# Optimization experiments

Hardware: AMD Instinct MI355X
Metric: run time of the kernel (lower is better)

The kernel has to match this reference:

```python
import jax, jax.numpy as jnp
import numpy as np

K = 9  # knn kernel_size
SLOPE = 0.01  # LeakyReLU slope inside EdgeConv MLP (PyGraphBipartite default)


def setup_inputs() -> dict:
    key = jax.random.key(0)
    ks = jax.random.split(key, 5)
    B, C, H, W = 8, 96, 64, 64
    x = jax.random.normal(ks[0], (B, C, H, W), dtype=jnp.float32)
    # EdgeConv MLP: Linear(2C -> C), LeakyReLU(0.01), Linear(C -> C)
    W1 = jax.random.normal(ks[1], (2 * C, C), dtype=jnp.float32) * (1.0 / np.sqrt(2 * C))
    b1 = jax.random.normal(ks[2], (C,), dtype=jnp.float32) * 0.01
    W2 = jax.random.normal(ks[3], (C, C), dtype=jnp.float32) * (1.0 / np.sqrt(C))
    b2 = jax.random.normal(ks[4], (C,), dtype=jnp.float32) * 0.01
    return {"x": x, "W1": W1, "b1": b1, "W2": W2, "b2": b2}


def reference(x, W1, b1, W2, b2):
    B, C, H, W = x.shape
    M = H * W
    # flat_nodes: (B,C,H,W) -> per-image node features (B, M, C)
    xf = jnp.transpose(x, (0, 2, 3, 1)).reshape(B, M, C)

    # k-NN graph per image (batch-restricted), loop=True so self is a neighbor (dist 0)
    sq = jnp.sum(xf * xf, axis=-1)  # (B, M)
    dist = sq[:, :, None] + sq[:, None, :] - 2.0 * jnp.einsum("bmc,bnc->bmn", xf, xf)
    _, idx = jax.lax.top_k(-dist, K)  # (B, M, K) neighbor indices per center node

    # gather neighbor features: (B, M, K, C)
    xj = jax.vmap(lambda f, i: f[i])(xf, idx)
    xi = xf[:, :, None, :]  # center node, broadcast over K

    # EdgeConv message: MLP([x_i ; x_j - x_i]), then mean over neighbors
    feat = jnp.concatenate([jnp.broadcast_to(xi, xj.shape), xj - xi], axis=-1)  # (B,M,K,2C)
    h = feat @ W1 + b1
    h = jnp.where(h >= 0, h, SLOPE * h)  # LeakyReLU(0.01)
    h = h @ W2 + b2  # (B, M, K, C)
    out = jnp.mean(h, axis=2)  # mean aggregation -> (B, M, C)

    # norm='none' (Identity), act='relu'
    out = jax.nn.relu(out)

    # unflat_nodes: (B, M, C) -> (B, C, H, W)
    return jnp.transpose(out.reshape(B, H, W, C), (0, 3, 1, 2))
```

## Files before the change

### kernel.cpp

```cpp
#include <hip/hip_runtime.h>

#define B_ 8
#define C_ 96
#define CP_ 104
#define M_ 4096
#define K_ 9
#define NSPLIT 2
#define NPART (M_ / NSPLIT)
#define NTILES (NPART / 64)

typedef _Float16 f16x8 __attribute__((ext_vector_type(8)));
typedef float f32x4 __attribute__((ext_vector_type(4)));

#define INSERT(dv, nv) do {                                                   \
    const int pz_ = tpos;                                                     \
    _Pragma("unroll")                                                         \
    for (int k_ = 0; k_ < K_; ++k_) if (k_ == pz_) { tv[k_] = (dv); ti[k_] = (nv); } \
    float mx_ = tv[0]; int mp_ = 0;                                           \
    _Pragma("unroll")                                                         \
    for (int k_ = 1; k_ < K_; ++k_) if (tv[k_] > mx_) { mx_ = tv[k_]; mp_ = k_; } \
    tmax = mx_; tpos = mp_;                                                   \
  } while (0)

__global__ __launch_bounds__(256) void prep1_kernel(
    const float* __restrict__ x, float* __restrict__ sq,
    unsigned short* __restrict__ xhi, unsigned short* __restrict__ xlo) {
  __shared__ float Xt[C_][64];
  const int b = blockIdx.y, m0 = blockIdx.x * 64, tid = threadIdx.x;
  const float* xb = x + (size_t)b * C_ * M_;
  for (int i = tid; i < C_ * 16; i += 256) {
    int c = i >> 4, j4 = (i & 15) << 2;
    *(float4*)&Xt[c][j4] = *(const float4*)&xb[(size_t)c * M_ + m0 + j4];
  }
  __syncthreads();
  if (tid < 64) {
    float s = 0.f;
#pragma unroll
    for (int c = 0; c < C_; ++c) { float v = Xt[c][tid]; s += v * v; }
    sq[b * M_ + m0 + tid] = s;
  }
  const int p = tid & 63, part = tid >> 6;
  union { unsigned short u[24]; uint4 q[3]; } hb, lb;
#pragma unroll
  for (int i = 0; i < 24; ++i) {
    float v = Xt[part * 24 + i][p];
    _Float16 h = (_Float16)v;
    _Float16 l = (_Float16)(v - (float)h);
    hb.u[i] = __builtin_bit_cast(unsigned short, h);
    lb.u[i] = __builtin_bit_cast(unsigned short, l);
  }
  size_t base = ((size_t)b * M_ + m0 + p) * CP_ + part * 24;
#pragma unroll
  for (int i = 0; i < 3; ++i) {
    *(uint4*)&xhi[base + i * 8] = hb.q[i];
    *(uint4*)&xlo[base + i * 8] = lb.q[i];
  }
}

__global__ __launch_bounds__(256, 3) void knn_kernel(
    const unsigned short* __restrict__ xhi, const unsigned short* __restrict__ xlo,
    const float* __restrict__ sq, float* __restrict__ pv, int* __restrict__ pi) {
  __shared__ struct { unsigned short bhi[64 * CP_]; unsigned short blo[64 * CP_]; } S;
  __shared__ float sqc[64];
  const int b = blockIdx.y, r0 = blockIdx.x * 64, h = blockIdx.z;
  const int tid = threadIdx.x;
  const int lane = tid & 63, w = tid >> 6;
  const int fp = lane & 15, kg = lane >> 4;
  const size_t bm = (size_t)b * M_;
  const int nbeg = h * NPART;

  f16x8 qhi[3], qlo[3];
#pragma unroll
  for (int kt = 0; kt < 3; ++kt) {
    size_t off = (bm + r0 + w * 16 + fp) * CP_ + kt * 32 + kg * 8;
    qhi[kt] = *(const f16x8*)&xhi[off];
    qlo[kt] = *(const f16x8*)&xlo[off];
  }

  float tv[K_]; int ti[K_]; float tmax = 3.4e38f; int tpos = 0;
#pragma unroll
  for (int k = 0; k < K_; ++k) { tv[k] = 3.4e38f; ti[k] = 0; }

  uint4 ph0, ph1, ph2, ph3, pl0, pl1, pl2, pl3;
  float sqreg = 0.f;
  auto gload = [&](int n0) {
    const uint4* gh = (const uint4*)(xhi + (bm + n0) * CP_);
    const uint4* gl = (const uint4*)(xlo + (bm + n0) * CP_);
    ph0 = gh[tid]; ph1 = gh[tid + 256]; ph2 = gh[tid + 512];
    pl0 = gl[tid]; pl1 = gl[tid + 256]; pl2 = gl[tid + 512];
    if (tid < 64) {
      ph3 = gh[tid + 768]; pl3 = gl[tid + 768];
      sqreg = sq[bm + n0 + tid];
    }
  };
  auto swrite = [&]() {
    uint4* dh = (uint4*)S.bhi; uint4* dl = (uint4*)S.blo;
    dh[tid] = ph0; dh[tid + 256] = ph1; dh[tid + 512] = ph2;
    dl[tid] = pl0; dl[tid + 256] = pl1; dl[tid + 512] = pl2;
    if (tid < 64) { dh[tid + 768] = ph3; dl[tid + 768] = pl3; sqc[tid] = sqreg; }
  };

  gload(nbeg);
  for (int t = 0; t < NTILES; ++t) {
    const int n0 = nbeg + t * 64;
    __syncthreads();
    swrite();
    if (t < NTILES - 1) gload(n0 + 64);
    __syncthreads();

    float b0d = 0.f, b1d = 0.f; int b0n = 0, b1n = 0, bcnt = 0;

#pragma unroll
    for (int rs = 0; rs < 4; ++rs) {
      f16x8 nh[3], nl[3];
#pragma unroll
      for (int kt = 0; kt < 3; ++kt) {
        int boff = (rs * 16 + fp) * CP_ + kt * 32 + kg * 8;
        nh[kt] = *(const f16x8*)&S.bhi[boff];
        nl[kt] = *(const f16x8*)&S.blo[boff];
      }
      f32x4 acc = {0.f, 0.f, 0.f, 0.f};
#pragma unroll
      for (int kt = 0; kt < 3; ++kt) {
        acc = __builtin_amdgcn_mfma_f32_16x16x32_f16(nh[kt], qhi[kt], acc, 0, 0, 0);
        acc = __builtin_amdgcn_mfma_f32_16x16x32_f16(nh[kt], qlo[kt], acc, 0, 0, 0);
        acc = __builtin_amdgcn_mfma_f32_16x16x32_f16(nl[kt], qhi[kt], acc, 0, 0, 0);
      }
#pragma unroll
      for (int r = 0; r < 4; ++r) {
        const int nrow = rs * 16 + kg * 4 + r;
        const float d = sqc[nrow] - 2.f * acc[r];
        if (d < tmax) {
          const int n = n0 + nrow;
          if (bcnt == 2) {
            if (b0d < tmax) INSERT(b0d, b0n);
            b0d = b1d; b0n = b1n;
            b1d = d;   b1n = n;
          } else if (bcnt == 1) {
            b1d = d; b1n = n; bcnt = 2;
          } else {
            b0d = d; b0n = n; bcnt = 1;
          }
        }
      }
    }
    if (bcnt >= 1 && b0d < tmax) INSERT(b0d, b0n);
    if (bcnt == 2 && b1d < tmax) INSERT(b1d, b1n);
  }

  __syncthreads();
  float* mv = (float*)&S;
  int*   mi = (int*)((char*)&S + 64 * 37 * 4);
  const int qrow = w * 16 + fp;
#pragma unroll
  for (int k = 0; k < K_; ++k) {
    mv[qrow * 37 + kg * K_ + k] = tv[k];
    mi[qrow * 37 + kg * K_ + k] = ti[k];
  }
  __syncthreads();
  if (tid < 64) {
    float fv[K_]; int fi[K_];
    float mx = 3.4e38f; int mp = 0;
#pragma unroll
    for (int k = 0; k < K_; ++k) { fv[k] = 3.4e38f; fi[k] = 0; }
    for (int s = 0; s < 36; ++s) {
      float v = mv[tid * 37 + s]; int id = mi[tid * 37 + s];
      if (v < mx) {
#pragma unroll
        for (int k = 0; k < K_; ++k) if (k == mp) { fv[k] = v; fi[k] = id; }
        float m2 = fv[0]; int p2 = 0;
#pragma unroll
        for (int k = 1; k < K_; ++k) if (fv[k] > m2) { m2 = fv[k]; p2 = k; }
        mx = m2; mp = p2;
      }
    }
    size_t base = ((size_t)h * B_ * M_ + bm + r0 + tid) * K_;
#pragma unroll
    for (int k = 0; k < K_; ++k) { pv[base + k] = fv[k]; pi[base + k] = fi[k]; }
  }
}

__global__ __launch_bounds__(256) void knn_merge_kernel(
    const float* __restrict__ pv, const int* __restrict__ pi,
    int* __restrict__ idxw) {
  const int g = blockIdx.x * 256 + threadIdx.x;
  float tv[K_]; int ti[K_]; float tmax = 3.4e38f; int tpos = 0;
#pragma unroll
  for (int k = 0; k < K_; ++k) { tv[k] = 3.4e38f; ti[k] = 0; }
#pragma unroll
  for (int h = 0; h < NSPLIT; ++h) {
    const float* vs = pv + ((size_t)h * B_ * M_ + g) * K_;
    const int*   is = pi + ((size_t)h * B_ * M_ + g) * K_;
#pragma unroll
    for (int s = 0; s < K_; ++s) {
      float d = vs[s];
      if (d < tmax) { int n = is[s]; INSERT(d, n); }
    }
  }
#pragma unroll
  for (int k = 0; k < K_; ++k) idxw[(size_t)g * K_ + k] = ti[k];
}

__global__ __launch_bounds__(256) void prep2_kernel(
    const float* __restrict__ x, const float* __restrict__ W1,
    const float* __restrict__ b1, float* __restrict__ P, float* __restrict__ Q) {
  __shared__ float Xt[C_][64];
  __shared__ float Wt[C_][64];
  const int b = blockIdx.y, m0 = blockIdx.x * 64;
  const int tid = threadIdx.x;
  const float* xb = x + (size_t)b * C_ * M_;

  for (int i = tid; i < C_ * 16; i += 256) {
    int c = i >> 4, j4 = (i & 15) << 2;
    *(float4*)&Xt[c][j4] = *(const float4*)&xb[(size_t)c * M_ + m0 + j4];
  }

  const int ty = tid >> 4, tx = tid & 15;
  for (int t = 0; t < 3; ++t) {
    const int u0 = t * 64;
    __syncthreads();
    for (int i = tid; i < C_ * 64; i += 256) {
      int cin = i >> 6, j = i & 63;
      int u = u0 + j;
      float wv;
      if (u < C_) wv = W1[cin * C_ + u] - W1[(C_ + cin) * C_ + u];
      else        wv = W1[(C_ + cin) * C_ + (u - C_)];
      Wt[cin][j] = wv;
    }
    __syncthreads();
    float acc[4][4] = {};
#pragma unroll 8
    for (int c = 0; c < C_; ++c) {
      float4 rr = *(const float4*)&Xt[c][ty << 2];
      float4 ww = *(const float4*)&Wt[c][tx << 2];
      acc[0][0] += rr.x * ww.x; acc[0][1] += rr.x * ww.y; acc[0][2] += rr.x * ww.z; acc[0][3] += rr.x * ww.w;
      acc[1][0] += rr.y * ww.x; acc[1][1] += rr.y * ww.y; acc[1][2] += rr.y * ww.z; acc[1][3] += rr.y * ww.w;
      acc[2][0] += rr.z * ww.x; acc[2][1] += rr.z * ww.y; acc[2][2] += rr.z * ww.z; acc[2][3] += rr.z * ww.w;
      acc[3][0] += rr.w * ww.x; acc[3][1] += rr.w * ww.y; acc[3][2] += rr.w * ww.z; acc[3][3] += rr.w * ww.w;
    }
#pragma unroll
    for (int i = 0; i < 4; ++i) {
      int m = m0 + (ty << 2) + i;
      size_t base = ((size_t)b * M_ + m) * C_;
#pragma unroll
      for (int j = 0; j < 4; ++j) {
        int u = u0 + (tx << 2) + j;
        float v = acc[i][j];
        if (u < C_) P[base + u] = v + b1[u];
        else        Q[base + (u - C_)] = v;
      }
    }
  }
}

__global__ __launch_bounds__(256) void edge_mlp_kernel(
    const float* __restrict__ P, const float* __restrict__ Q,
    const int* __restrict__ idxw, const float* __restrict__ W2,
    const float* __restrict__ b2, float* __restrict__ out) {
  __shared__ float g_l[C_][64];
  __shared__ float W2t[C_ * C_];
  const int b = blockIdx.y, m0 = blockIdx.x * 64;
  const int tid = threadIdx.x;

  for (int i = tid; i < (C_ * C_) / 4; i += 256)
    *(float4*)&W2t[i * 4] = *(const float4*)&W2[i * 4];

  const int ml = tid & 63, cg = tid >> 6;
  const int m = m0 + ml;
  const float* prow = P + ((size_t)b * M_ + m) * C_ + cg * 24;
  float pr[24];
#pragma unroll
  for (int t = 0; t < 24; t += 4) {
    float4 v = *(const float4*)(prow + t);
    pr[t] = v.x; pr[t + 1] = v.y; pr[t + 2] = v.z; pr[t + 3] = v.w;
  }
  float gacc[24] = {};
  const int* irow = idxw + ((size_t)b * M_ + m) * K_;
#pragma unroll
  for (int k = 0; k < K_; ++k) {
    int j = irow[k];
    const float* qrow = Q + ((size_t)b * M_ + j) * C_ + cg * 24;
#pragma unroll
    for (int t = 0; t < 24; t += 4) {
      float4 qv = *(const float4*)(qrow + t);
      float h;
      h = pr[t + 0] + qv.x; gacc[t + 0] += (h >= 0.f) ? h : 0.01f * h;
      h = pr[t + 1] + qv.y; gacc[t + 1] += (h >= 0.f) ? h : 0.01f * h;
      h = pr[t + 2] + qv.z; gacc[t + 2] += (h >= 0.f) ? h : 0.01f * h;
      h = pr[t + 3] + qv.w; gacc[t + 3] += (h >= 0.f) ? h : 0.01f * h;
    }
  }
#pragma unroll
  for (int t = 0; t < 24; ++t) g_l[cg * 24 + t][ml] = gacc[t] * (1.f / 9.f);
  __syncthreads();

  const int ty = tid >> 4, tx = tid & 15;
  float acc2[4][6] = {};
#pragma unroll 4
  for (int c = 0; c < C_; ++c) {
    float4 rr = *(const float4*)&g_l[c][ty << 2];
    float2 wa = *(const float2*)&W2t[c * C_ + tx * 6];
    float2 wb = *(const float2*)&W2t[c * C_ + tx * 6 + 2];
    float2 wc = *(const float2*)&W2t[c * C_ + tx * 6 + 4];
    float rv[4] = {rr.x, rr.y, rr.z, rr.w};
    float wv[6] = {wa.x, wa.y, wb.x, wb.y, wc.x, wc.y};
#pragma unroll
    for (int i = 0; i < 4; ++i)
#pragma unroll
      for (int j = 0; j < 6; ++j) acc2[i][j] += rv[i] * wv[j];
  }
#pragma unroll
  for (int i = 0; i < 4; ++i) {
    int mm = m0 + (ty << 2) + i;
#pragma unroll
    for (int j = 0; j < 6; ++j) {
      int u = tx * 6 + j;
      float v = acc2[i][j] + b2[u];
      v = fmaxf(v, 0.f);
      out[((size_t)b * C_ + u) * M_ + mm] = v;
    }
  }
}

extern "C" void kernel_launch(void* const* d_in, const int* in_sizes, int n_in,
                              void* d_out, int out_size, void* d_ws, size_t ws_size,
                              hipStream_t stream) {
  const float* x  = (const float*)d_in[0];
  const float* W1 = (const float*)d_in[1];
  const float* b1 = (const float*)d_in[2];
  const float* W2 = (const float*)d_in[3];
  const float* b2 = (const float*)d_in[4];
  float* out = (float*)d_out;

  char* ws = (char*)d_ws;
  float* sq  = (float*)ws;
  int* idxw  = (int*)(ws + 131072);
  unsigned short* xhi = (unsigned short*)(ws + 1310720);
  unsigned short* xlo = (unsigned short*)(ws + 8126464);
  float* pv = (float*)(ws + 14942208);
  int*   pi = (int*)(ws + 19660800);
  float* P = (float*)(ws + 1310720);
  float* Q = (float*)(ws + 13893632);

  dim3 blk(256);
  prep1_kernel<<<dim3(M_ / 64, B_), blk, 0, stream>>>(x, sq, xhi, xlo);
  knn_kernel<<<dim3(M_ / 64, B_, NSPLIT), blk, 0, stream>>>(xhi, xlo, sq, pv, pi);
  knn_merge_kernel<<<dim3(B_ * M_ / 256), blk, 0, stream>>>(pv, pi, idxw);
  prep2_kernel<<<dim3(M_ / 64, B_), blk, 0, stream>>>(x, W1, b1, P, Q);
  edge_mlp_kernel<<<dim3(M_ / 64, B_), blk, 0, stream>>>(P, Q, idxw, W2, b2, out);
}
```

Before: 278.5 us.

## Split kNN candidate range four ways and use branchless top-2 filtering per tile

Splits the candidate range into four parts instead of two, which doubles the block count for the distance/top-k kernel and raises parallelism. Each tile's per-row selection is also reworked: every lane branchlessly tracks its two smallest distances and counts how many fall below the current threshold. Only when some lane has more than two qualifying candidates does the wave fall back to full insertion over the stored distances. This cuts divergent insertion work in the common case, at the cost of more partial lists to merge and extra registers for the 16 stored distances.

```diff
diff --git a/kernel.cpp b/kernel.cpp
--- a/kernel.cpp
+++ b/kernel.cpp
@@ -5,7 +5,7 @@
 #define CP_ 104
 #define M_ 4096
 #define K_ 9
-#define NSPLIT 2
+#define NSPLIT 4
 #define NPART (M_ / NSPLIT)
 #define NTILES (NPART / 64)
 
@@ -108,7 +108,10 @@
     if (t < NTILES - 1) gload(n0 + 64);
     __syncthreads();
 
-    float b0d = 0.f, b1d = 0.f; int b0n = 0, b1n = 0, bcnt = 0;
+    const float t0 = tmax;
+    float s0 = 3.4e38f, s1 = 3.4e38f;
+    int i0 = 0, i1 = 0, cnt = 0;
+    float dstore[16];
 
 #pragma unroll
     for (int rs = 0; rs < 4; ++rs) {
@@ -129,23 +132,35 @@
 #pragma unroll
       for (int r = 0; r < 4; ++r) {
         const int nrow = rs * 16 + kg * 4 + r;
+        const int n = n0 + nrow;
         const float d = sqc[nrow] - 2.f * acc[r];
+        dstore[rs * 4 + r] = d;
+        cnt += (d < t0) ? 1 : 0;
+        const bool c0 = d < s0;
+        const float mx = fmaxf(s0, d);
+        const int i0o = i0;
+        s0 = fminf(s0, d);
+        i0 = c0 ? n : i0;
+        const int cmx = c0 ? i0o : n;
+        const bool c1 = mx < s1;
+        s1 = fminf(s1, mx);
+        i1 = c1 ? cmx : i1;
+      }
+    }
+
+    if (__any(cnt > 2)) {
+#pragma unroll
+      for (int j = 0; j < 16; ++j) {
+        const float d = dstore[j];
         if (d < tmax) {
-          const int n = n0 + nrow;
-          if (bcnt == 2) {
-            if (b0d < tmax) INSERT(b0d, b0n);
-            b0d = b1d; b0n = b1n;
-            b1d = d;   b1n = n;
-          } else if (bcnt == 1) {
-            b1d = d; b1n = n; bcnt = 2;
-          } else {
-            b0d = d; b0n = n; bcnt = 1;
-          }
+          const int n = n0 + (j >> 2) * 16 + kg * 4 + (j & 3);
+          INSERT(d, n);
         }
       }
-    }
-    if (bcnt >= 1 && b0d < tmax) INSERT(b0d, b0n);
-    if (bcnt == 2 && b1d < tmax) INSERT(b1d, b1n);
+    } else {
+      if (s0 < tmax) { INSERT(s0, i0); }
+      if (s1 < tmax) { INSERT(s1, i1); }
+    }
   }
 
   __syncthreads();
```

Result: slower. 350.1 us (+25.7%).
